# Kernel tuning notes

Measured on AMD Instinct MI355X. Metric: run time of the kernel, lower is better.

The kernel has to match this reference:

```python
import jax, jax.numpy as jnp
import numpy as np

DT = 0.01
NUM_STEPS = 2
DIM = 8        # latentDim (q:4, p:4)
HID = 128      # hiddenDim
BATCH = 524288


def _hamiltonian(z, W1, b1, W2, b2, W3, b3):
    # MLP H: (batch, 8) -> (batch,) scalar energy, tanh activations
    h = jnp.tanh(z @ W1 + b1)
    h = jnp.tanh(h @ W2 + b2)
    return (h @ W3 + b3)[..., 0]


def _grad_h(z, W1, b1, W2, b2, W3, b3):
    # dH/dz, batched; mirrors torch.autograd.grad(H.sum(), z)
    # torch detaches z before grad (create_graph keeps param graph)
    zc = jax.lax.stop_gradient(z)
    return jax.grad(lambda zz: _hamiltonian(zz, W1, b1, W2, b2, W3, b3).sum())(zc)


def setup_inputs() -> dict:
    key = jax.random.key(0)
    ks = jax.random.split(key, 7)
    z = jax.random.normal(ks[0], (BATCH, DIM), dtype=jnp.float32)
    W1 = jax.random.normal(ks[1], (DIM, HID), dtype=jnp.float32) / np.float32(np.sqrt(DIM))
    b1 = jnp.zeros((HID,), dtype=jnp.float32)
    W2 = jax.random.normal(ks[2], (HID, HID), dtype=jnp.float32) / np.float32(np.sqrt(HID))
    b2 = jnp.zeros((HID,), dtype=jnp.float32)
    W3 = jax.random.normal(ks[3], (HID, 1), dtype=jnp.float32) / np.float32(np.sqrt(HID))
    b3 = jnp.zeros((1,), dtype=jnp.float32)
    return {"z": z, "W1": W1, "b1": b1, "W2": W2, "b2": b2, "W3": W3, "b3": b3}


def reference(z, W1, b1, W2, b2, W3, b3):
    q, p = jnp.split(z, 2, axis=1)
    for _ in range(NUM_STEPS):
        g = _grad_h(jnp.concatenate([q, p], axis=1), W1, b1, W2, b2, W3, b3)
        dHdq, dHdp = jnp.split(g, 2, axis=1)
        p_half = p - 0.5 * DT * dHdq
        q_new = q + DT * dHdp
        g2 = _grad_h(jnp.concatenate([q_new, p_half], axis=1), W1, b1, W2, b2, W3, b3)
        dHdq_new = jnp.split(g2, 2, axis=1)[0]
        p = p_half - 0.5 * DT * dHdq_new
        q = q_new
    return jnp.concatenate([q, p], axis=1)
```

## Files before the change

### kernel.cpp

```cpp
#include <hip/hip_runtime.h>


typedef float f32x4 __attribute__((ext_vector_type(4)));
typedef int   i32x2 __attribute__((ext_vector_type(2)));
typedef int   i32x4 __attribute__((ext_vector_type(4)));
typedef int   i32x8 __attribute__((ext_vector_type(8)));

#define DT 0.01f
#define S1 64.0f
#define TWO_LOG2E 2.8853900817779268f
#define SCL1 0x7F7F7F7F

#define OFF_W1B 0
#define OFF_W2B 4096
#define OFF_W2T 20480
#define OFF_W1T 36864
#define WTOT    38912

__device__ __forceinline__ unsigned char to_fp8(float x) {
    return (unsigned char)(__builtin_amdgcn_cvt_pk_fp8_f32(x, x, 0, false) & 0xff);
}
__device__ __forceinline__ float fexp2(float x) {
#if __has_builtin(__builtin_amdgcn_exp2f)
    return __builtin_amdgcn_exp2f(x);
#else
    return exp2f(x);
#endif
}
__device__ __forceinline__ float frcp(float x) {
#if __has_builtin(__builtin_amdgcn_rcpf)
    return __builtin_amdgcn_rcpf(x);
#else
    return 1.0f / x;
#endif
}

__device__ __forceinline__ i32x2 tr8(unsigned char* p) {
#if __has_builtin(__builtin_amdgcn_ds_read_tr8_b64)
    return __builtin_amdgcn_ds_read_tr8_b64((__attribute__((address_space(3))) i32x2*)p);
#else
    i32x2 d;
    asm volatile("ds_read_b64_tr_b8 %0, %1\n\ts_waitcnt lgkmcnt(0)"
                 : "=v"(d)
                 : "v"((unsigned)(unsigned long long)(__attribute__((address_space(3))) void*)p)
                 : "memory");
    __builtin_amdgcn_sched_barrier(0);
    return d;
#endif
}

__device__ __forceinline__ i32x8 cat44(i32x4 a, i32x4 b) {
    return __builtin_shufflevector(a, b, 0, 1, 2, 3, 4, 5, 6, 7);
}

__device__ __forceinline__ i32x8 read_a(unsigned char* abase) {
    i32x2 a0 = tr8(abase);
    i32x2 a1 = tr8(abase + 512);
    i32x2 a2 = tr8(abase + 1024);
    i32x2 a3 = tr8(abase + 1536);
    i32x4 lo = __builtin_shufflevector(a0, a1, 0, 1, 2, 3);
    i32x4 hi = __builtin_shufflevector(a2, a3, 0, 1, 2, 3);
    return cat44(lo, hi);
}

__device__ __forceinline__ f32x4 mm128(i32x8 a, i32x8 b, f32x4 c) {
#if __has_builtin(__builtin_amdgcn_mfma_scale_f32_16x16x128_f8f6f4)
    return __builtin_amdgcn_mfma_scale_f32_16x16x128_f8f6f4(a, b, c, 0, 0, 0, SCL1, 0, SCL1);
#else
    #pragma unroll
    for (int kt = 0; kt < 4; kt++) {
        long long aa = ((long long)(unsigned)a[2 * kt + 1] << 32) | (unsigned)a[2 * kt];
        long long bb = ((long long)(unsigned)b[2 * kt + 1] << 32) | (unsigned)b[2 * kt];
        c = __builtin_amdgcn_mfma_f32_16x16x32_fp8_fp8(aa, bb, c, 0, 0, 0);
    }
    return c;
#endif
}

__global__ __launch_bounds__(256) void hnn_prep_kernel(
    const float* __restrict__ W1, const float* __restrict__ W2,
    const float* __restrict__ W3, unsigned char* __restrict__ ws)
{
    const int t = threadIdx.x, b = blockIdx.x;
    if (b == 0) {
        for (int i = t; i < 1024; i += 256) ((int*)(ws + OFF_W1B))[i] = 0;
        for (int i = t; i < 512;  i += 256) ((int*)(ws + OFF_W1T))[i] = 0;
        __syncthreads();
        for (int i = t; i < 1024; i += 256) {
            int row = i >> 7, col = i & 127;
            float w = W1[i];
            ws[OFF_W1B + (col >> 4) * 512 + (col & 15) * 8 + row] = to_fp8(w * TWO_LOG2E);
            int c = col >> 5, h = c >> 1, s = (c & 1) * 8 + (col & 7);
            int qd = (col >> 3) & 3;
            ws[OFF_W1T + (h * 64 + qd * 16 + row) * 16 + s] = to_fp8(w);
        }
    } else {
        int idx = (b - 1) * 256 + t;
        int row = idx >> 7, col = idx & 127;
        float w = W2[idx];
        {
            int c = row >> 5, h = c >> 1, s = (c & 1) * 8 + (row & 7);
            int qd = (row >> 3) & 3;
            ws[OFF_W2B + (((col >> 4) * 2 + h) * 64 + qd * 16 + (col & 15)) * 16 + s] =
                to_fp8(w * TWO_LOG2E);
        }
        {
            int c = col >> 5, h = c >> 1, s = (c & 1) * 8 + (col & 7);
            int qd = (col >> 3) & 3;
            ws[OFF_W2T + (((row >> 4) * 2 + h) * 64 + qd * 16 + (row & 15)) * 16 + s] =
                to_fp8(w * 256.0f * W3[col]);
        }
    }
}

__global__ __launch_bounds__(512) void hnn_leapfrog_kernel(
    const float* __restrict__ Z, const unsigned char* __restrict__ WS,
    const float* __restrict__ B1f, const float* __restrict__ B2f,
    float* __restrict__ OUT)
{
    __shared__ __align__(16) unsigned char sWT[WTOT];
    __shared__ __align__(16) unsigned char sACT[8 * 2048];
    __shared__ __align__(16) float sZ[1024];

    const int t   = threadIdx.x;
    const int blk = blockIdx.x;

    for (int i = t; i < WTOT / 16; i += 512)
        __builtin_amdgcn_global_load_lds(
            (const __attribute__((address_space(1))) void*)(WS + i * 16),
            (__attribute__((address_space(3))) void*)(sWT + i * 16), 16, 0, 0);
    sZ[t]       = Z[blk * 1024 + t];
    sZ[t + 512] = Z[blk * 1024 + 512 + t];

    const int lane = t & 63;
    const int wv   = t >> 6;
    const int nn   = lane & 15;
    const int qd   = lane >> 4;

    float eb1v[8], eb2v[8];
    #pragma unroll
    for (int nt = 0; nt < 8; nt++) {
        eb1v[nt] = fexp2(B1f[nt * 16 + nn] * TWO_LOG2E);
        eb2v[nt] = fexp2(B2f[nt * 16 + nn] * TWO_LOG2E);
    }
    __syncthreads();

    unsigned char* act   = sACT + wv * 2048;
    float*         zrow  = sZ + wv * 128;
    unsigned char* abase = act + qd * 128 + nn;
    unsigned char* awr   = act + nn * 16 + qd * 4;
    const unsigned char* w8  = sWT + lane * 8;
    const unsigned char* w16 = sWT + lane * 16;

    const f32x4 zc = {0.f, 0.f, 0.f, 0.f};

    #pragma unroll 1
    for (int ev = 0; ev < 4; ev++) {
        long long az = 0;
        if (qd == 0) {
            const f32x4* zr = (const f32x4*)(zrow + nn * 8);
            f32x4 z0 = zr[0], z1 = zr[1];
            int lo = __builtin_amdgcn_cvt_pk_fp8_f32(z0[0], z0[1], 0, false);
            lo     = __builtin_amdgcn_cvt_pk_fp8_f32(z0[2], z0[3], lo, true);
            int hi = __builtin_amdgcn_cvt_pk_fp8_f32(z1[0], z1[1], 0, false);
            hi     = __builtin_amdgcn_cvt_pk_fp8_f32(z1[2], z1[3], hi, true);
            az = ((long long)(unsigned)hi << 32) | (unsigned)lo;
        }
        float hc[8][4];
        #pragma unroll
        for (int nt = 0; nt < 8; nt++) {
            long long bf = *(const long long*)(w8 + OFF_W1B + nt * 512);
            f32x4 c = __builtin_amdgcn_mfma_f32_16x16x32_fp8_fp8(az, bf, zc, 0, 0, 0);
            #pragma unroll
            for (int r = 0; r < 4; r++) {
                float e  = fexp2(c[r]);
                float rr = frcp(fmaf(e, eb1v[nt], 1.0f));
                hc[nt][r] = fmaf(-2.0f, rr, 1.0f);
            }
            int v = __builtin_amdgcn_cvt_pk_fp8_f32(hc[nt][0], hc[nt][1], 0, false);
            v     = __builtin_amdgcn_cvt_pk_fp8_f32(hc[nt][2], hc[nt][3], v, true);
            *(int*)(awr + nt * 256) = v;
        }
        i32x8 a8 = read_a(abase);
        #pragma unroll
        for (int nt = 0; nt < 8; nt++) {
            i32x4 bA = *(const i32x4*)(w16 + OFF_W2B + nt * 2048);
            i32x4 bB = *(const i32x4*)(w16 + OFF_W2B + nt * 2048 + 1024);
            f32x4 c = mm128(a8, cat44(bA, bB), zc);
            float dd[4];
            #pragma unroll
            for (int r = 0; r < 4; r++) {
                float e  = fexp2(c[r]);
                float rr = frcp(fmaf(e, eb2v[nt], 1.0f));
                dd[r] = fmaf(-rr, rr, rr);
            }
            int v = __builtin_amdgcn_cvt_pk_fp8_f32(dd[0], dd[1], 0, false);
            v     = __builtin_amdgcn_cvt_pk_fp8_f32(dd[2], dd[3], v, true);
            *(int*)(awr + nt * 256) = v;
        }
        a8 = read_a(abase);
        #pragma unroll
        for (int nt = 0; nt < 8; nt++) {
            i32x4 bA = *(const i32x4*)(w16 + OFF_W2T + nt * 2048);
            i32x4 bB = *(const i32x4*)(w16 + OFF_W2T + nt * 2048 + 1024);
            f32x4 c = mm128(a8, cat44(bA, bB), zc);
            float dd[4];
            #pragma unroll
            for (int r = 0; r < 4; r++) {
                float h = hc[nt][r];
                dd[r] = c[r] * fmaf(-h, h, 1.0f);
            }
            int v = __builtin_amdgcn_cvt_pk_fp8_f32(dd[0], dd[1], 0, false);
            v     = __builtin_amdgcn_cvt_pk_fp8_f32(dd[2], dd[3], v, true);
            *(int*)(awr + nt * 256) = v;
        }
        a8 = read_a(abase);
        i32x4 bA = *(const i32x4*)(w16 + OFF_W1T);
        i32x4 bB = *(const i32x4*)(w16 + OFF_W1T + 1024);
        f32x4 g = mm128(a8, cat44(bA, bB), zc);
        const bool first = (ev & 1) == 0;
        if (nn < 4) {
            float* p = zrow + qd * 32 + nn + 4;
            #pragma unroll
            for (int r = 0; r < 4; r++) p[r * 8] -= (0.5f * DT / S1) * g[r];
        } else if (nn < 8 && first) {
            float* p = zrow + qd * 32 + (nn - 4);
            #pragma unroll
            for (int r = 0; r < 4; r++) p[r * 8] += (DT / S1) * g[r];
        }
    }

    OUT[blk * 1024 + wv * 128 + lane]      = zrow[lane];
    OUT[blk * 1024 + wv * 128 + 64 + lane] = zrow[64 + lane];
}

extern "C" void kernel_launch(void* const* d_in, const int* in_sizes, int n_in,
                              void* d_out, int out_size, void* d_ws, size_t ws_size,
                              hipStream_t stream) {
    const float* Z  = (const float*)d_in[0];
    const float* W1 = (const float*)d_in[1];
    const float* B1 = (const float*)d_in[2];
    const float* W2 = (const float*)d_in[3];
    const float* B2 = (const float*)d_in[4];
    const float* W3 = (const float*)d_in[5];
    float* OUT = (float*)d_out;
    unsigned char* ws = (unsigned char*)d_ws;
    int blocks = in_sizes[0] / 1024;
    hipLaunchKernelGGL(hnn_prep_kernel, dim3(65), dim3(256), 0, stream, W1, W2, W3, ws);
    hipLaunchKernelGGL(hnn_leapfrog_kernel, dim3(blocks), dim3(512), 0, stream,
                       Z, ws, B1, B2, OUT);
}
```

Before: 240.2 us.

## Fuse weight prep into persistent grid-stride leapfrog kernel with seven waves per block

Drops the separate prep kernel. Each block of a persistent grid (768 blocks of 7 waves) now converts W1/W2/W3 to FP8 straight into LDS, then loops wave-independently over 128-float jobs. The W1 buffers are compacted to cut LDS use, and the launch overhead and workspace round trip go away. The trade-off is that every block redundantly reads and converts the full fp32 weights, and the grid-stride loop loads z per wave with no overlap.

```diff
diff --git a/kernel.cpp b/kernel.cpp
--- a/kernel.cpp
+++ b/kernel.cpp
@@ -1,6 +1,7 @@
 #include <hip/hip_runtime.h>
 
 
+typedef float f32x2 __attribute__((ext_vector_type(2)));
 typedef float f32x4 __attribute__((ext_vector_type(4)));
 typedef int   i32x2 __attribute__((ext_vector_type(2)));
 typedef int   i32x4 __attribute__((ext_vector_type(4)));
@@ -12,10 +13,10 @@
 #define SCL1 0x7F7F7F7F
 
 #define OFF_W1B 0
-#define OFF_W2B 4096
-#define OFF_W2T 20480
-#define OFF_W1T 36864
-#define WTOT    38912
+#define OFF_W2B 1024
+#define OFF_W2T 17408
+#define OFF_W1T 33792
+#define WTOT    34816
 
 __device__ __forceinline__ unsigned char to_fp8(float x) {
     return (unsigned char)(__builtin_amdgcn_cvt_pk_fp8_f32(x, x, 0, false) & 0xff);
@@ -77,60 +78,44 @@
 #endif
 }
 
-__global__ __launch_bounds__(256) void hnn_prep_kernel(
-    const float* __restrict__ W1, const float* __restrict__ W2,
-    const float* __restrict__ W3, unsigned char* __restrict__ ws)
+#define NWAVES 7
+
+__global__ __launch_bounds__(64 * NWAVES) void hnn_leapfrog_kernel(
+    const float* __restrict__ Z, const float* __restrict__ W1,
+    const float* __restrict__ B1f, const float* __restrict__ W2,
+    const float* __restrict__ B2f, const float* __restrict__ W3,
+    float* __restrict__ OUT, int njobs)
 {
-    const int t = threadIdx.x, b = blockIdx.x;
-    if (b == 0) {
-        for (int i = t; i < 1024; i += 256) ((int*)(ws + OFF_W1B))[i] = 0;
-        for (int i = t; i < 512;  i += 256) ((int*)(ws + OFF_W1T))[i] = 0;
-        __syncthreads();
-        for (int i = t; i < 1024; i += 256) {
-            int row = i >> 7, col = i & 127;
-            float w = W1[i];
-            ws[OFF_W1B + (col >> 4) * 512 + (col & 15) * 8 + row] = to_fp8(w * TWO_LOG2E);
-            int c = col >> 5, h = c >> 1, s = (c & 1) * 8 + (col & 7);
-            int qd = (col >> 3) & 3;
-            ws[OFF_W1T + (h * 64 + qd * 16 + row) * 16 + s] = to_fp8(w);
-        }
-    } else {
-        int idx = (b - 1) * 256 + t;
-        int row = idx >> 7, col = idx & 127;
-        float w = W2[idx];
+    __shared__ __align__(16) unsigned char sWT[WTOT];
+    __shared__ __align__(16) unsigned char sACT[NWAVES * 2048];
+    __shared__ __align__(16) float sZ[NWAVES * 128];
+
+    const int t = threadIdx.x;
+
+    for (int i = t; i < 1024; i += 64 * NWAVES) {
+        int row = i >> 7, col = i & 127;
+        float w = W1[i];
+        sWT[OFF_W1B + (col >> 4) * 128 + (col & 15) * 8 + row] = to_fp8(w * TWO_LOG2E);
+        int c = col >> 5, h = c >> 1, s = (c & 1) * 8 + (col & 7);
+        int qd2 = (col >> 3) & 3;
+        sWT[OFF_W1T + ((h * 4 + qd2) * 8 + row) * 16 + s] = to_fp8(w);
+    }
+    for (int i = t; i < 16384; i += 64 * NWAVES) {
+        int row = i >> 7, col = i & 127;
+        float w = W2[i];
         {
             int c = row >> 5, h = c >> 1, s = (c & 1) * 8 + (row & 7);
-            int qd = (row >> 3) & 3;
-            ws[OFF_W2B + (((col >> 4) * 2 + h) * 64 + qd * 16 + (col & 15)) * 16 + s] =
+            int qd2 = (row >> 3) & 3;
+            sWT[OFF_W2B + (((col >> 4) * 2 + h) * 64 + qd2 * 16 + (col & 15)) * 16 + s] =
                 to_fp8(w * TWO_LOG2E);
         }
         {
             int c = col >> 5, h = c >> 1, s = (c & 1) * 8 + (col & 7);
-            int qd = (col >> 3) & 3;
-            ws[OFF_W2T + (((row >> 4) * 2 + h) * 64 + qd * 16 + (row & 15)) * 16 + s] =
+            int qd2 = (col >> 3) & 3;
+            sWT[OFF_W2T + (((row >> 4) * 2 + h) * 64 + qd2 * 16 + (row & 15)) * 16 + s] =
                 to_fp8(w * 256.0f * W3[col]);
         }
     }
-}
-
-__global__ __launch_bounds__(512) void hnn_leapfrog_kernel(
-    const float* __restrict__ Z, const unsigned char* __restrict__ WS,
-    const float* __restrict__ B1f, const float* __restrict__ B2f,
-    float* __restrict__ OUT)
-{
-    __shared__ __align__(16) unsigned char sWT[WTOT];
-    __shared__ __align__(16) unsigned char sACT[8 * 2048];
-    __shared__ __align__(16) float sZ[1024];
-
-    const int t   = threadIdx.x;
-    const int blk = blockIdx.x;
-
-    for (int i = t; i < WTOT / 16; i += 512)
-        __builtin_amdgcn_global_load_lds(
-            (const __attribute__((address_space(1))) void*)(WS + i * 16),
-            (__attribute__((address_space(3))) void*)(sWT + i * 16), 16, 0, 0);
-    sZ[t]       = Z[blk * 1024 + t];
-    sZ[t + 512] = Z[blk * 1024 + 512 + t];
 
     const int lane = t & 63;
     const int wv   = t >> 6;
@@ -149,89 +134,97 @@
     float*         zrow  = sZ + wv * 128;
     unsigned char* abase = act + qd * 128 + nn;
     unsigned char* awr   = act + nn * 16 + qd * 4;
-    const unsigned char* w8  = sWT + lane * 8;
-    const unsigned char* w16 = sWT + lane * 16;
+    const unsigned char* w1b  = sWT + OFF_W1B + nn * 8;
+    const unsigned char* w16  = sWT + lane * 16;
+    const unsigned char* w1t  = sWT + OFF_W1T + (qd * 8 + (nn & 7)) * 16;
 
     const f32x4 zc = {0.f, 0.f, 0.f, 0.f};
+    const int stride = gridDim.x * NWAVES;
 
     #pragma unroll 1
-    for (int ev = 0; ev < 4; ev++) {
-        long long az = 0;
-        if (qd == 0) {
-            const f32x4* zr = (const f32x4*)(zrow + nn * 8);
-            f32x4 z0 = zr[0], z1 = zr[1];
-            int lo = __builtin_amdgcn_cvt_pk_fp8_f32(z0[0], z0[1], 0, false);
-            lo     = __builtin_amdgcn_cvt_pk_fp8_f32(z0[2], z0[3], lo, true);
-            int hi = __builtin_amdgcn_cvt_pk_fp8_f32(z1[0], z1[1], 0, false);
-            hi     = __builtin_amdgcn_cvt_pk_fp8_f32(z1[2], z1[3], hi, true);
-            az = ((long long)(unsigned)hi << 32) | (unsigned)lo;
+    for (int job = blockIdx.x * NWAVES + wv; job < njobs; job += stride) {
+        f32x2 zv = ((const f32x2*)(Z + job * 128))[lane];
+        ((f32x2*)zrow)[lane] = zv;
+
+        #pragma unroll 1
+        for (int ev = 0; ev < 4; ev++) {
+            long long az = 0;
+            if (qd == 0) {
+                const f32x4* zr = (const f32x4*)(zrow + nn * 8);
+                f32x4 z0 = zr[0], z1 = zr[1];
+                int lo = __builtin_amdgcn_cvt_pk_fp8_f32(z0[0], z0[1], 0, false);
+                lo     = __builtin_amdgcn_cvt_pk_fp8_f32(z0[2], z0[3], lo, true);
+                int hi = __builtin_amdgcn_cvt_pk_fp8_f32(z1[0], z1[1], 0, false);
+                hi     = __builtin_amdgcn_cvt_pk_fp8_f32(z1[2], z1[3], hi, true);
+                az = ((long long)(unsigned)hi << 32) | (unsigned)lo;
+            }
+            float hc[8][4];
+            #pragma unroll
+            for (int nt = 0; nt < 8; nt++) {
+                long long bf = *(const long long*)(w1b + nt * 128);
+                f32x4 c = __builtin_amdgcn_mfma_f32_16x16x32_fp8_fp8(az, bf, zc, 0, 0, 0);
+                #pragma unroll
+                for (int r = 0; r < 4; r++) {
+                    float e  = fexp2(c[r]);
+                    float rr = frcp(fmaf(e, eb1v[nt], 1.0f));
+                    hc[nt][r] = fmaf(-2.0f, rr, 1.0f);
+                }
+                int v = __builtin_amdgcn_cvt_pk_fp8_f32(hc[nt][0], hc[nt][1], 0, false);
+                v     = __builtin_amdgcn_cvt_pk_fp8_f32(hc[nt][2], hc[nt][3], v, true);
+                *(int*)(awr + nt * 256) = v;
+            }
+            i32x8 a8 = read_a(abase);
+            #pragma unroll
+            for (int nt = 0; nt < 8; nt++) {
+                i32x4 bA = *(const i32x4*)(w16 + OFF_W2B + nt * 2048);
+                i32x4 bB = *(const i32x4*)(w16 + OFF_W2B + nt * 2048 + 1024);
+                f32x4 c = mm128(a8, cat44(bA, bB), zc);
+                float dd[4];
+                #pragma unroll
+                for (int r = 0; r < 4; r++) {
+                    float e  = fexp2(c[r]);
+                    float rr = frcp(fmaf(e, eb2v[nt], 1.0f));
+                    dd[r] = fmaf(-rr, rr, rr);
+                }
+                int v = __builtin_amdgcn_cvt_pk_fp8_f32(dd[0], dd[1], 0, false);
+                v     = __builtin_amdgcn_cvt_pk_fp8_f32(dd[2], dd[3], v, true);
+                *(int*)(awr + nt * 256) = v;
+            }
+            a8 = read_a(abase);
+            #pragma unroll
+            for (int nt = 0; nt < 8; nt++) {
+                i32x4 bA = *(const i32x4*)(w16 + OFF_W2T + nt * 2048);
+                i32x4 bB = *(const i32x4*)(w16 + OFF_W2T + nt * 2048 + 1024);
+                f32x4 c = mm128(a8, cat44(bA, bB), zc);
+                float dd[4];
+                #pragma unroll
+                for (int r = 0; r < 4; r++) {
+                    float h = hc[nt][r];
+                    dd[r] = c[r] * fmaf(-h, h, 1.0f);
+                }
+                int v = __builtin_amdgcn_cvt_pk_fp8_f32(dd[0], dd[1], 0, false);
+                v     = __builtin_amdgcn_cvt_pk_fp8_f32(dd[2], dd[3], v, true);
+                *(int*)(awr + nt * 256) = v;
+            }
+            a8 = read_a(abase);
+            i32x4 bA = *(const i32x4*)(w1t);
+            i32x4 bB = *(const i32x4*)(w1t + 512);
+            f32x4 g = mm128(a8, cat44(bA, bB), zc);
+            const bool first = (ev & 1) == 0;
+            if (nn < 4) {
+                float* p = zrow + qd * 32 + nn + 4;
+                #pragma unroll
+                for (int r = 0; r < 4; r++) p[r * 8] -= (0.5f * DT / S1) * g[r];
+            } else if (nn < 8 && first) {
+                float* p = zrow + qd * 32 + (nn - 4);
+                #pragma unroll
+                for (int r = 0; r < 4; r++) p[r * 8] += (DT / S1) * g[r];
+            }
         }
-        float hc[8][4];
-        #pragma unroll
-        for (int nt = 0; nt < 8; nt++) {
-            long long bf = *(const long long*)(w8 + OFF_W1B + nt * 512);
-            f32x4 c = __builtin_amdgcn_mfma_f32_16x16x32_fp8_fp8(az, bf, zc, 0, 0, 0);
-            #pragma unroll
-            for (int r = 0; r < 4; r++) {
-                float e  = fexp2(c[r]);
-                float rr = frcp(fmaf(e, eb1v[nt], 1.0f));
-                hc[nt][r] = fmaf(-2.0f, rr, 1.0f);
-            }
-            int v = __builtin_amdgcn_cvt_pk_fp8_f32(hc[nt][0], hc[nt][1], 0, false);
-            v     = __builtin_amdgcn_cvt_pk_fp8_f32(hc[nt][2], hc[nt][3], v, true);
-            *(int*)(awr + nt * 256) = v;
-        }
-        i32x8 a8 = read_a(abase);
-        #pragma unroll
-        for (int nt = 0; nt < 8; nt++) {
-            i32x4 bA = *(const i32x4*)(w16 + OFF_W2B + nt * 2048);
-            i32x4 bB = *(const i32x4*)(w16 + OFF_W2B + nt * 2048 + 1024);
-            f32x4 c = mm128(a8, cat44(bA, bB), zc);
-            float dd[4];
-            #pragma unroll
-            for (int r = 0; r < 4; r++) {
-                float e  = fexp2(c[r]);
-                float rr = frcp(fmaf(e, eb2v[nt], 1.0f));
-                dd[r] = fmaf(-rr, rr, rr);
-            }
-            int v = __builtin_amdgcn_cvt_pk_fp8_f32(dd[0], dd[1], 0, false);
-            v     = __builtin_amdgcn_cvt_pk_fp8_f32(dd[2], dd[3], v, true);
-            *(int*)(awr + nt * 256) = v;
-        }
-        a8 = read_a(abase);
-        #pragma unroll
-        for (int nt = 0; nt < 8; nt++) {
-            i32x4 bA = *(const i32x4*)(w16 + OFF_W2T + nt * 2048);
-            i32x4 bB = *(const i32x4*)(w16 + OFF_W2T + nt * 2048 + 1024);
-            f32x4 c = mm128(a8, cat44(bA, bB), zc);
-            float dd[4];
-            #pragma unroll
-            for (int r = 0; r < 4; r++) {
-                float h = hc[nt][r];
-                dd[r] = c[r] * fmaf(-h, h, 1.0f);
-            }
-            int v = __builtin_amdgcn_cvt_pk_fp8_f32(dd[0], dd[1], 0, false);
-            v     = __builtin_amdgcn_cvt_pk_fp8_f32(dd[2], dd[3], v, true);
-            *(int*)(awr + nt * 256) = v;
-        }
-        a8 = read_a(abase);
-        i32x4 bA = *(const i32x4*)(w16 + OFF_W1T);
-        i32x4 bB = *(const i32x4*)(w16 + OFF_W1T + 1024);
-        f32x4 g = mm128(a8, cat44(bA, bB), zc);
-        const bool first = (ev & 1) == 0;
-        if (nn < 4) {
-            float* p = zrow + qd * 32 + nn + 4;
-            #pragma unroll
-            for (int r = 0; r < 4; r++) p[r * 8] -= (0.5f * DT / S1) * g[r];
-        } else if (nn < 8 && first) {
-            float* p = zrow + qd * 32 + (nn - 4);
-            #pragma unroll
-            for (int r = 0; r < 4; r++) p[r * 8] += (DT / S1) * g[r];
-        }
-    }
-
-    OUT[blk * 1024 + wv * 128 + lane]      = zrow[lane];
-    OUT[blk * 1024 + wv * 128 + 64 + lane] = zrow[64 + lane];
+
+        OUT[job * 128 + lane]      = zrow[lane];
+        OUT[job * 128 + 64 + lane] = zrow[64 + lane];
+    }
 }
 
 extern "C" void kernel_launch(void* const* d_in, const int* in_sizes, int n_in,
@@ -244,9 +237,10 @@
     const float* B2 = (const float*)d_in[4];
     const float* W3 = (const float*)d_in[5];
     float* OUT = (float*)d_out;
-    unsigned char* ws = (unsigned char*)d_ws;
-    int blocks = in_sizes[0] / 1024;
-    hipLaunchKernelGGL(hnn_prep_kernel, dim3(65), dim3(256), 0, stream, W1, W2, W3, ws);
-    hipLaunchKernelGGL(hnn_leapfrog_kernel, dim3(blocks), dim3(512), 0, stream,
-                       Z, ws, B1, B2, OUT);
-}
+    int njobs = in_sizes[0] / 128;
+    int grid  = 256 * 3;
+    int maxg  = (njobs + NWAVES - 1) / NWAVES;
+    if (grid > maxg) grid = maxg;
+    hipLaunchKernelGGL(hnn_leapfrog_kernel, dim3(grid), dim3(64 * NWAVES), 0, stream,
+                       Z, W1, B1, W2, B2, W3, OUT, njobs);
+}
```

Result: slower. 285.1 us (+18.7%).
